# Kernel tuning notes

Measured on AMD Instinct MI355X. Metric: run time of the kernel, lower is better.

## Reference

```python
import jax, jax.numpy as jnp
import numpy as np

# dims: batch B, seq T, d_model C, expert_hidden H, n_experts E (top-1 routing)
B, T, C, H, E = 1, 256, 1024, 2048, 8
STD = 0.02


def setup_inputs() -> dict:
    key = jax.random.key(0)
    ks = jax.random.split(key, 8)
    f32 = jnp.float32
    return {
        "x": jax.random.normal(ks[0], (B, T, C), f32),
        "up": jax.random.normal(ks[1], (E, H, C), f32) * STD,
        "gate": jax.random.normal(ks[2], (E, H, C), f32) * STD,
        "down": jax.random.normal(ks[3], (E, C, H), f32) * STD,
        "router": jax.random.normal(ks[4], (E, C), f32) * STD,
        "w_up_s": jax.random.normal(ks[5], (H, C), f32) * STD,
        "w_gate_s": jax.random.normal(ks[6], (H, C), f32) * STD,
        "w_down_s": jax.random.normal(ks[7], (C, H), f32) * STD,
    }


def reference(x, up, gate, down, router, w_up_s, w_gate_s, w_down_s):
    b, t, c = x.shape
    x_ = x.reshape(b * t, c)                      # [BT, C]
    # top-1 router (gates are implicitly 1.0)
    logits = x_ @ router.T                        # [BT, E]
    idx = jnp.argmax(logits, axis=-1)             # [BT]
    onehot = jax.nn.one_hot(idx, router.shape[0], dtype=x.dtype)  # [BT, E]
    # dense all-expert SwiGLU, combined with one-hot (same math as per-token gather)
    u = jnp.einsum('bc,ehc->ebh', x_, up)         # [E, BT, H]
    g = jnp.einsum('bc,ehc->ebh', x_, gate)       # [E, BT, H]
    h = jax.nn.silu(g) * u                        # [E, BT, H]
    ye = jnp.einsum('ebh,ech->ebc', h, down)      # [E, BT, C]
    y = jnp.einsum('ebc,be->bc', ye, onehot)      # [BT, C]
    # shared expert residual
    ys = (jax.nn.silu(x_ @ w_gate_s.T) * (x_ @ w_up_s.T)) @ w_down_s.T
    return (y + ys).reshape(b, t, c)
```

## Files before the change

### kernel.cpp

```cpp
#include <hip/hip_runtime.h>
#include <hip/hip_bf16.h>

#define T_TOK 256
#define C_DIM 1024
#define H_DIM 2048
#define E_NUM 8
#define BN 64

typedef __attribute__((ext_vector_type(4))) float f32x4;
typedef __attribute__((ext_vector_type(8))) short short8;

#define WS_IDX   0
#define WS_CNT   1024
#define WS_LIST  2048
#define WS_HBUF  16384
#define WS_HSBUF (16384 + 1048576)
#define WS_YS    (16384 + 2*1048576)

__device__ __forceinline__ ushort f2bf(float f) {
    __hip_bfloat16 h = __float2bfloat16(f);
    return *reinterpret_cast<ushort*>(&h);
}

__device__ __forceinline__ short8 pack8(float4 a, float4 b) {
    short8 s;
    s[0] = (short)f2bf(a.x); s[1] = (short)f2bf(a.y);
    s[2] = (short)f2bf(a.z); s[3] = (short)f2bf(a.w);
    s[4] = (short)f2bf(b.x); s[5] = (short)f2bf(b.y);
    s[6] = (short)f2bf(b.z); s[7] = (short)f2bf(b.w);
    return s;
}

__global__ __launch_bounds__(256) void router_kernel(
    const float* __restrict__ x, const float* __restrict__ router,
    int* __restrict__ idx, int* __restrict__ cnt, int* __restrict__ list)
{
    const int t = blockIdx.x;
    const int tid = threadIdx.x;
    float4 xv = reinterpret_cast<const float4*>(x + (size_t)t * C_DIM)[tid];
    float p[E_NUM];
#pragma unroll
    for (int e = 0; e < E_NUM; e++) {
        float4 rv = reinterpret_cast<const float4*>(router + (size_t)e * C_DIM)[tid];
        p[e] = xv.x * rv.x + xv.y * rv.y + xv.z * rv.z + xv.w * rv.w;
    }
#pragma unroll
    for (int e = 0; e < E_NUM; e++) {
#pragma unroll
        for (int off = 32; off >= 1; off >>= 1)
            p[e] += __shfl_down(p[e], off, 64);
    }
    __shared__ float red[E_NUM][4];
    const int lane = tid & 63, wv = tid >> 6;
    if (lane == 0) {
#pragma unroll
        for (int e = 0; e < E_NUM; e++) red[e][wv] = p[e];
    }
    __syncthreads();
    if (tid == 0) {
        float best = -3.4e38f; int bi = 0;
#pragma unroll
        for (int e = 0; e < E_NUM; e++) {
            float v = red[e][0] + red[e][1] + red[e][2] + red[e][3];
            if (v > best) { best = v; bi = e; }
        }
        idx[t] = bi;
        int pos = atomicAdd(&cnt[bi], 1);
        list[bi * T_TOK + pos] = t;
    }
}

__global__ __launch_bounds__(256, 3) void ug_mfma(
    const float* __restrict__ x, const float* __restrict__ up, const float* __restrict__ gate,
    const float* __restrict__ w_up_s, const float* __restrict__ w_gate_s,
    const int* __restrict__ cnt, const int* __restrict__ list,
    ushort* __restrict__ hbuf, ushort* __restrict__ hsbuf)
{
    const int e = blockIdx.x;
    const bool sh = (e == E_NUM);
    const int n = sh ? T_TOK : cnt[e];
    const int tg0 = blockIdx.z * 64;
    if (tg0 >= n) return;

    const int tid = threadIdx.x;
    const int lane = tid & 63, wv = tid >> 6;

    __shared__ ushort Ax[64][72];
    __shared__ ushort Wu[64][72];
    __shared__ ushort Wg[64][72];
    __shared__ int toks_s[64];
    if (tid < 64) {
        int t = tg0 + tid;
        toks_s[tid] = (t < n) ? (sh ? t : list[e * T_TOK + t]) : -1;
    }
    __syncthreads();

    const int srow = tid >> 2;
    const int sseg = (tid & 3) * 16;
    const float* __restrict__ pu = (sh ? w_up_s   : up   + (size_t)e * H_DIM * C_DIM)
                                   + (size_t)(blockIdx.y * BN + srow) * C_DIM + sseg;
    const float* __restrict__ pg = (sh ? w_gate_s : gate + (size_t)e * H_DIM * C_DIM)
                                   + (size_t)(blockIdx.y * BN + srow) * C_DIM + sseg;
    const int stok = toks_s[srow];
    const float* __restrict__ px = x + (size_t)(stok < 0 ? 0 : stok) * C_DIM + sseg;

    float4 ru[4], rg[4], rx[4];
#define UG_LOAD(kc) do { \
        _Pragma("unroll") \
        for (int i = 0; i < 4; i++) { \
            ru[i] = *reinterpret_cast<const float4*>(pu + (kc) + i * 4); \
            rg[i] = *reinterpret_cast<const float4*>(pg + (kc) + i * 4); \
            rx[i] = (stok >= 0) ? *reinterpret_cast<const float4*>(px + (kc) + i * 4) \
                                : float4{0.f, 0.f, 0.f, 0.f}; \
        } \
    } while (0)

    const int klane = (lane >> 4) * 8;
    const int mrow = lane & 15;
    f32x4 au[4] = {{0,0,0,0},{0,0,0,0},{0,0,0,0},{0,0,0,0}};
    f32x4 ag[4] = {{0,0,0,0},{0,0,0,0},{0,0,0,0},{0,0,0,0}};

    UG_LOAD(0);
#pragma unroll 1
    for (int t = 0; t < 16; t++) {
        __syncthreads();
        *reinterpret_cast<short8*>(&Wu[srow][sseg])     = pack8(ru[0], ru[1]);
        *reinterpret_cast<short8*>(&Wu[srow][sseg + 8]) = pack8(ru[2], ru[3]);
        *reinterpret_cast<short8*>(&Wg[srow][sseg])     = pack8(rg[0], rg[1]);
        *reinterpret_cast<short8*>(&Wg[srow][sseg + 8]) = pack8(rg[2], rg[3]);
        *reinterpret_cast<short8*>(&Ax[srow][sseg])     = pack8(rx[0], rx[1]);
        *reinterpret_cast<short8*>(&Ax[srow][sseg + 8]) = pack8(rx[2], rx[3]);
        __syncthreads();
        if (t < 15) UG_LOAD((t + 1) * 64);
#pragma unroll
        for (int k0 = 0; k0 < 64; k0 += 32) {
            short8 bu = *reinterpret_cast<const short8*>(&Wu[wv * 16 + mrow][klane + k0]);
            short8 bg = *reinterpret_cast<const short8*>(&Wg[wv * 16 + mrow][klane + k0]);
#pragma unroll
            for (int mf = 0; mf < 4; mf++) {
                short8 a = *reinterpret_cast<const short8*>(&Ax[mf * 16 + mrow][klane + k0]);
                au[mf] = __builtin_amdgcn_mfma_f32_16x16x32_bf16(a, bu, au[mf], 0, 0, 0);
                ag[mf] = __builtin_amdgcn_mfma_f32_16x16x32_bf16(a, bg, ag[mf], 0, 0, 0);
            }
        }
    }
#undef UG_LOAD

    const int hglob = blockIdx.y * BN + wv * 16 + mrow;
    ushort* __restrict__ outp = sh ? hsbuf : hbuf;
#pragma unroll
    for (int mf = 0; mf < 4; mf++) {
#pragma unroll
        for (int r = 0; r < 4; r++) {
            int m = mf * 16 + (lane >> 4) * 4 + r;
            int tok = toks_s[m];
            if (tok >= 0) {
                float g = ag[mf][r], u = au[mf][r];
                float hv = u * (g / (1.f + __expf(-g)));
                outp[(size_t)tok * H_DIM + hglob] = f2bf(hv);
            }
        }
    }
}

__global__ __launch_bounds__(256, 4) void down_mfma(
    const float* __restrict__ dwn, const float* __restrict__ w_down_s,
    const ushort* __restrict__ hbuf, const ushort* __restrict__ hsbuf,
    const int* __restrict__ cnt, const int* __restrict__ list,
    float* __restrict__ y, float* __restrict__ ysbuf)
{
    const int e = blockIdx.x;
    const bool sh = (e == E_NUM);
    const int n = sh ? T_TOK : cnt[e];
    const int tg0 = blockIdx.z * 32;
    if (tg0 >= n) return;

    const int tid = threadIdx.x;
    const int lane = tid & 63, wv = tid >> 6;

    __shared__ ushort Ah[32][72];
    __shared__ ushort Wd[64][72];
    __shared__ int toks_s[32];
    if (tid < 32) {
        int t = tg0 + tid;
        toks_s[tid] = (t < n) ? (sh ? t : list[e * T_TOK + t]) : -1;
    }
    __syncthreads();

    const int srow = tid >> 2;
    const int sseg = (tid & 3) * 16;
    const float* __restrict__ pd = (sh ? w_down_s : dwn + (size_t)e * C_DIM * H_DIM)
                                   + (size_t)(blockIdx.y * BN + srow) * H_DIM + sseg;
    const int hrow = tid >> 3;
    const int hseg = (tid & 7) * 8;
    const int stok = toks_s[hrow];
    const ushort* __restrict__ hin = sh ? hsbuf : hbuf;
    const ushort* __restrict__ ph = hin + (size_t)(stok < 0 ? 0 : stok) * H_DIM + hseg;

    float4 rd[4]; short8 rh;
#define DN_LOAD(kc) do { \
        _Pragma("unroll") \
        for (int i = 0; i < 4; i++) \
            rd[i] = *reinterpret_cast<const float4*>(pd + (kc) + i * 4); \
        rh = (stok >= 0) ? *reinterpret_cast<const short8*>(ph + (kc)) \
                         : short8{0,0,0,0,0,0,0,0}; \
    } while (0)

    const int klane = (lane >> 4) * 8;
    const int mrow = lane & 15;
    f32x4 acc[2] = {{0,0,0,0},{0,0,0,0}};

    DN_LOAD(0);
#pragma unroll 1
    for (int t = 0; t < 32; t++) {
        __syncthreads();
        *reinterpret_cast<short8*>(&Wd[srow][sseg])     = pack8(rd[0], rd[1]);
        *reinterpret_cast<short8*>(&Wd[srow][sseg + 8]) = pack8(rd[2], rd[3]);
        *reinterpret_cast<short8*>(&Ah[hrow][hseg])     = rh;
        __syncthreads();
        if (t < 31) DN_LOAD((t + 1) * 64);
#pragma unroll
        for (int k0 = 0; k0 < 64; k0 += 32) {
            short8 bd = *reinterpret_cast<const short8*>(&Wd[wv * 16 + mrow][klane + k0]);
#pragma unroll
            for (int mf = 0; mf < 2; mf++) {
                short8 a = *reinterpret_cast<const short8*>(&Ah[mf * 16 + mrow][klane + k0]);
                acc[mf] = __builtin_amdgcn_mfma_f32_16x16x32_bf16(a, bd, acc[mf], 0, 0, 0);
            }
        }
    }
#undef DN_LOAD

    const int cglob = blockIdx.y * BN + wv * 16 + mrow;
    float* __restrict__ outp = sh ? ysbuf : y;
#pragma unroll
    for (int mf = 0; mf < 2; mf++) {
#pragma unroll
        for (int r = 0; r < 4; r++) {
            int m = mf * 16 + (lane >> 4) * 4 + r;
            int tok = toks_s[m];
            if (tok >= 0) outp[(size_t)tok * C_DIM + cglob] = acc[mf][r];
        }
    }
}

__global__ __launch_bounds__(256) void add_kernel(float* __restrict__ y, const float* __restrict__ ys)
{
    int i = blockIdx.x * 256 + threadIdx.x;
    float4 a = reinterpret_cast<float4*>(y)[i];
    float4 b = reinterpret_cast<const float4*>(ys)[i];
    a.x += b.x; a.y += b.y; a.z += b.z; a.w += b.w;
    reinterpret_cast<float4*>(y)[i] = a;
}

extern "C" void kernel_launch(void* const* d_in, const int* in_sizes, int n_in,
                              void* d_out, int out_size, void* d_ws, size_t ws_size,
                              hipStream_t stream)
{
    const float* x        = (const float*)d_in[0];
    const float* up       = (const float*)d_in[1];
    const float* gate     = (const float*)d_in[2];
    const float* dwn      = (const float*)d_in[3];
    const float* router   = (const float*)d_in[4];
    const float* w_up_s   = (const float*)d_in[5];
    const float* w_gate_s = (const float*)d_in[6];
    const float* w_down_s = (const float*)d_in[7];

    char* ws = (char*)d_ws;
    int* idx     = (int*)(ws + WS_IDX);
    int* cnt     = (int*)(ws + WS_CNT);
    int* list    = (int*)(ws + WS_LIST);
    ushort* hbuf  = (ushort*)(ws + WS_HBUF);
    ushort* hsbuf = (ushort*)(ws + WS_HSBUF);
    float* ysbuf  = (float*)(ws + WS_YS);
    float* y = (float*)d_out;

    hipMemsetAsync(cnt, 0, E_NUM * sizeof(int), stream);
    router_kernel<<<T_TOK, 256, 0, stream>>>(x, router, idx, cnt, list);
    ug_mfma<<<dim3(E_NUM + 1, H_DIM / BN, 4), 256, 0, stream>>>(
        x, up, gate, w_up_s, w_gate_s, cnt, list, hbuf, hsbuf);
    down_mfma<<<dim3(E_NUM + 1, C_DIM / BN, 8), 256, 0, stream>>>(
        dwn, w_down_s, hbuf, hsbuf, cnt, list, y, ysbuf);
    add_kernel<<<(T_TOK * C_DIM / 4) / 256, 256, 0, stream>>>(y, ysbuf);
}
```

Before: 101.5 us.

## Replace LDS-tiled MoE GEMMs with split-K direct-register MFMA and pre-converted bf16 activations

The router kernel now also writes a bf16 copy of x, so the up/gate GEMM no longer converts activations on every tile. Both expert GEMMs drop the LDS-staged, double-synchronised 64-wide tiles. Each block now covers 16 output columns by 32 tokens, with its four waves splitting K and loading operands straight from global memory into MFMA registers. The partial sums are then reduced through LDS. This gives far more blocks and removes the per-step barriers, at the cost of reading weights once per 32-token group and losing LDS reuse of activations.

```diff
diff --git a/kernel.cpp b/kernel.cpp
--- a/kernel.cpp
+++ b/kernel.cpp
@@ -5,17 +5,16 @@
 #define C_DIM 1024
 #define H_DIM 2048
 #define E_NUM 8
-#define BN 64
 
 typedef __attribute__((ext_vector_type(4))) float f32x4;
 typedef __attribute__((ext_vector_type(8))) short short8;
 
-#define WS_IDX   0
-#define WS_CNT   1024
-#define WS_LIST  2048
-#define WS_HBUF  16384
-#define WS_HSBUF (16384 + 1048576)
-#define WS_YS    (16384 + 2*1048576)
+#define WS_CNT    0
+#define WS_LIST   1024
+#define WS_XBF    16384
+#define WS_HBUF   (1u<<20)
+#define WS_HSBUF  (2u<<20)
+#define WS_YS     (3u<<20)
 
 __device__ __forceinline__ ushort f2bf(float f) {
     __hip_bfloat16 h = __float2bfloat16(f);
@@ -31,13 +30,19 @@
     return s;
 }
 
+#define MFMA(a, b, c) __builtin_amdgcn_mfma_f32_16x16x32_bf16((a), (b), (c), 0, 0, 0)
+
 __global__ __launch_bounds__(256) void router_kernel(
     const float* __restrict__ x, const float* __restrict__ router,
-    int* __restrict__ idx, int* __restrict__ cnt, int* __restrict__ list)
+    int* __restrict__ cnt, int* __restrict__ list, ushort* __restrict__ xbf)
 {
     const int t = blockIdx.x;
     const int tid = threadIdx.x;
     float4 xv = reinterpret_cast<const float4*>(x + (size_t)t * C_DIM)[tid];
+    ushort4 xb;
+    xb.x = f2bf(xv.x); xb.y = f2bf(xv.y); xb.z = f2bf(xv.z); xb.w = f2bf(xv.w);
+    *reinterpret_cast<ushort4*>(xbf + (size_t)t * C_DIM + tid * 4) = xb;
+
     float p[E_NUM];
 #pragma unroll
     for (int e = 0; e < E_NUM; e++) {
@@ -64,100 +69,86 @@
             float v = red[e][0] + red[e][1] + red[e][2] + red[e][3];
             if (v > best) { best = v; bi = e; }
         }
-        idx[t] = bi;
         int pos = atomicAdd(&cnt[bi], 1);
         list[bi * T_TOK + pos] = t;
     }
 }
 
-__global__ __launch_bounds__(256, 3) void ug_mfma(
-    const float* __restrict__ x, const float* __restrict__ up, const float* __restrict__ gate,
+__global__ __launch_bounds__(256, 4) void ug_mfma(
+    const ushort* __restrict__ xbf, const float* __restrict__ up, const float* __restrict__ gate,
     const float* __restrict__ w_up_s, const float* __restrict__ w_gate_s,
     const int* __restrict__ cnt, const int* __restrict__ list,
     ushort* __restrict__ hbuf, ushort* __restrict__ hsbuf)
 {
-    const int e = blockIdx.x;
+    const int e = blockIdx.x, by = blockIdx.y, tt = blockIdx.z;
     const bool sh = (e == E_NUM);
     const int n = sh ? T_TOK : cnt[e];
-    const int tg0 = blockIdx.z * 64;
-    if (tg0 >= n) return;
-
-    const int tid = threadIdx.x;
-    const int lane = tid & 63, wv = tid >> 6;
-
-    __shared__ ushort Ax[64][72];
-    __shared__ ushort Wu[64][72];
-    __shared__ ushort Wg[64][72];
-    __shared__ int toks_s[64];
-    if (tid < 64) {
-        int t = tg0 + tid;
+    if (tt * 32 >= n) return;
+    const int tid = threadIdx.x, lane = tid & 63, wv = tid >> 6;
+    const int col = lane & 15, kg = lane >> 4, kl = kg * 8;
+
+    __shared__ float red[4][2][64][4];
+    __shared__ int toks_s[32];
+    if (tid < 32) {
+        int t = tt * 32 + tid;
         toks_s[tid] = (t < n) ? (sh ? t : list[e * T_TOK + t]) : -1;
     }
     __syncthreads();
 
-    const int srow = tid >> 2;
-    const int sseg = (tid & 3) * 16;
+    const int h0 = by * 16;
+    const int kb = wv * 256;
     const float* __restrict__ pu = (sh ? w_up_s   : up   + (size_t)e * H_DIM * C_DIM)
-                                   + (size_t)(blockIdx.y * BN + srow) * C_DIM + sseg;
+                                   + (size_t)(h0 + col) * C_DIM + kb + kl;
     const float* __restrict__ pg = (sh ? w_gate_s : gate + (size_t)e * H_DIM * C_DIM)
-                                   + (size_t)(blockIdx.y * BN + srow) * C_DIM + sseg;
-    const int stok = toks_s[srow];
-    const float* __restrict__ px = x + (size_t)(stok < 0 ? 0 : stok) * C_DIM + sseg;
-
-    float4 ru[4], rg[4], rx[4];
-#define UG_LOAD(kc) do { \
-        _Pragma("unroll") \
-        for (int i = 0; i < 4; i++) { \
-            ru[i] = *reinterpret_cast<const float4*>(pu + (kc) + i * 4); \
-            rg[i] = *reinterpret_cast<const float4*>(pg + (kc) + i * 4); \
-            rx[i] = (stok >= 0) ? *reinterpret_cast<const float4*>(px + (kc) + i * 4) \
-                                : float4{0.f, 0.f, 0.f, 0.f}; \
-        } \
-    } while (0)
-
-    const int klane = (lane >> 4) * 8;
-    const int mrow = lane & 15;
-    f32x4 au[4] = {{0,0,0,0},{0,0,0,0},{0,0,0,0},{0,0,0,0}};
-    f32x4 ag[4] = {{0,0,0,0},{0,0,0,0},{0,0,0,0},{0,0,0,0}};
-
-    UG_LOAD(0);
-#pragma unroll 1
-    for (int t = 0; t < 16; t++) {
-        __syncthreads();
-        *reinterpret_cast<short8*>(&Wu[srow][sseg])     = pack8(ru[0], ru[1]);
-        *reinterpret_cast<short8*>(&Wu[srow][sseg + 8]) = pack8(ru[2], ru[3]);
-        *reinterpret_cast<short8*>(&Wg[srow][sseg])     = pack8(rg[0], rg[1]);
-        *reinterpret_cast<short8*>(&Wg[srow][sseg + 8]) = pack8(rg[2], rg[3]);
-        *reinterpret_cast<short8*>(&Ax[srow][sseg])     = pack8(rx[0], rx[1]);
-        *reinterpret_cast<short8*>(&Ax[srow][sseg + 8]) = pack8(rx[2], rx[3]);
-        __syncthreads();
-        if (t < 15) UG_LOAD((t + 1) * 64);
-#pragma unroll
-        for (int k0 = 0; k0 < 64; k0 += 32) {
-            short8 bu = *reinterpret_cast<const short8*>(&Wu[wv * 16 + mrow][klane + k0]);
-            short8 bg = *reinterpret_cast<const short8*>(&Wg[wv * 16 + mrow][klane + k0]);
-#pragma unroll
-            for (int mf = 0; mf < 4; mf++) {
-                short8 a = *reinterpret_cast<const short8*>(&Ax[mf * 16 + mrow][klane + k0]);
-                au[mf] = __builtin_amdgcn_mfma_f32_16x16x32_bf16(a, bu, au[mf], 0, 0, 0);
-                ag[mf] = __builtin_amdgcn_mfma_f32_16x16x32_bf16(a, bg, ag[mf], 0, 0, 0);
-            }
-        }
-    }
-#undef UG_LOAD
-
-    const int hglob = blockIdx.y * BN + wv * 16 + mrow;
-    ushort* __restrict__ outp = sh ? hsbuf : hbuf;
-#pragma unroll
-    for (int mf = 0; mf < 4; mf++) {
-#pragma unroll
-        for (int r = 0; r < 4; r++) {
-            int m = mf * 16 + (lane >> 4) * 4 + r;
-            int tok = toks_s[m];
+                                   + (size_t)(h0 + col) * C_DIM + kb + kl;
+    const int t0 = toks_s[col], t1 = toks_s[16 + col];
+    const ushort* __restrict__ pa0 = xbf + (size_t)(t0 < 0 ? 0 : t0) * C_DIM + kb + kl;
+    const ushort* __restrict__ pa1 = xbf + (size_t)(t1 < 0 ? 0 : t1) * C_DIM + kb + kl;
+
+    f32x4 au0 = {0,0,0,0}, au1 = {0,0,0,0}, ag0 = {0,0,0,0}, ag1 = {0,0,0,0};
+#pragma unroll 4
+    for (int k = 0; k < 8; k++) {
+        const int o = k * 32;
+        short8 a0 = *reinterpret_cast<const short8*>(pa0 + o);
+        short8 a1 = *reinterpret_cast<const short8*>(pa1 + o);
+        float4 ua = *reinterpret_cast<const float4*>(pu + o);
+        float4 ub = *reinterpret_cast<const float4*>(pu + o + 4);
+        float4 ga = *reinterpret_cast<const float4*>(pg + o);
+        float4 gb = *reinterpret_cast<const float4*>(pg + o + 4);
+        short8 bu = pack8(ua, ub), bg = pack8(ga, gb);
+        au0 = MFMA(a0, bu, au0); au1 = MFMA(a1, bu, au1);
+        ag0 = MFMA(a0, bg, ag0); ag1 = MFMA(a1, bg, ag1);
+    }
+
+    *reinterpret_cast<f32x4*>(red[wv][0][lane]) = au0;
+    *reinterpret_cast<f32x4*>(red[wv][1][lane]) = au1;
+    __syncthreads();
+    f32x4 u4 = {0,0,0,0}, g4 = {0,0,0,0};
+    const int rv = (tid >> 6) & 1, rl = tid & 63;
+    if (tid < 128) {
+        u4 = *reinterpret_cast<const f32x4*>(red[0][rv][rl]);
+        u4 += *reinterpret_cast<const f32x4*>(red[1][rv][rl]);
+        u4 += *reinterpret_cast<const f32x4*>(red[2][rv][rl]);
+        u4 += *reinterpret_cast<const f32x4*>(red[3][rv][rl]);
+    }
+    __syncthreads();
+    *reinterpret_cast<f32x4*>(red[wv][0][lane]) = ag0;
+    *reinterpret_cast<f32x4*>(red[wv][1][lane]) = ag1;
+    __syncthreads();
+    if (tid < 128) {
+        g4 = *reinterpret_cast<const f32x4*>(red[0][rv][rl]);
+        g4 += *reinterpret_cast<const f32x4*>(red[1][rv][rl]);
+        g4 += *reinterpret_cast<const f32x4*>(red[2][rv][rl]);
+        g4 += *reinterpret_cast<const f32x4*>(red[3][rv][rl]);
+        ushort* __restrict__ outp = sh ? hsbuf : hbuf;
+#pragma unroll
+        for (int j = 0; j < 4; j++) {
+            int row = (rv ? 16 : 0) + (rl >> 4) * 4 + j;
+            int tok = toks_s[row];
             if (tok >= 0) {
-                float g = ag[mf][r], u = au[mf][r];
+                float g = g4[j], u = u4[j];
                 float hv = u * (g / (1.f + __expf(-g)));
-                outp[(size_t)tok * H_DIM + hglob] = f2bf(hv);
+                outp[(size_t)tok * H_DIM + h0 + (rl & 15)] = f2bf(hv);
             }
         }
     }
@@ -167,79 +158,61 @@
     const float* __restrict__ dwn, const float* __restrict__ w_down_s,
     const ushort* __restrict__ hbuf, const ushort* __restrict__ hsbuf,
     const int* __restrict__ cnt, const int* __restrict__ list,
-    float* __restrict__ y, float* __restrict__ ysbuf)
-{
-    const int e = blockIdx.x;
+    float* __restrict__ y, float* __restrict__ yspart)
+{
+    const int e = blockIdx.x, by = blockIdx.y, tt = blockIdx.z;
     const bool sh = (e == E_NUM);
     const int n = sh ? T_TOK : cnt[e];
-    const int tg0 = blockIdx.z * 32;
-    if (tg0 >= n) return;
-
-    const int tid = threadIdx.x;
-    const int lane = tid & 63, wv = tid >> 6;
-
-    __shared__ ushort Ah[32][72];
-    __shared__ ushort Wd[64][72];
+    if (tt * 32 >= n) return;
+    const int tid = threadIdx.x, lane = tid & 63, wv = tid >> 6;
+    const int col = lane & 15, kg = lane >> 4, kl = kg * 8;
+
+    __shared__ float red[4][2][64][4];
     __shared__ int toks_s[32];
     if (tid < 32) {
-        int t = tg0 + tid;
+        int t = tt * 32 + tid;
         toks_s[tid] = (t < n) ? (sh ? t : list[e * T_TOK + t]) : -1;
     }
     __syncthreads();
 
-    const int srow = tid >> 2;
-    const int sseg = (tid & 3) * 16;
+    const int c0 = by * 16;
+    const int kb = wv * 512;
     const float* __restrict__ pd = (sh ? w_down_s : dwn + (size_t)e * C_DIM * H_DIM)
-                                   + (size_t)(blockIdx.y * BN + srow) * H_DIM + sseg;
-    const int hrow = tid >> 3;
-    const int hseg = (tid & 7) * 8;
-    const int stok = toks_s[hrow];
+                                   + (size_t)(c0 + col) * H_DIM + kb + kl;
+    const int t0 = toks_s[col], t1 = toks_s[16 + col];
     const ushort* __restrict__ hin = sh ? hsbuf : hbuf;
-    const ushort* __restrict__ ph = hin + (size_t)(stok < 0 ? 0 : stok) * H_DIM + hseg;
-
-    float4 rd[4]; short8 rh;
-#define DN_LOAD(kc) do { \
-        _Pragma("unroll") \
-        for (int i = 0; i < 4; i++) \
-            rd[i] = *reinterpret_cast<const float4*>(pd + (kc) + i * 4); \
-        rh = (stok >= 0) ? *reinterpret_cast<const short8*>(ph + (kc)) \
-                         : short8{0,0,0,0,0,0,0,0}; \
-    } while (0)
-
-    const int klane = (lane >> 4) * 8;
-    const int mrow = lane & 15;
-    f32x4 acc[2] = {{0,0,0,0},{0,0,0,0}};
-
-    DN_LOAD(0);
-#pragma unroll 1
-    for (int t = 0; t < 32; t++) {
-        __syncthreads();
-        *reinterpret_cast<short8*>(&Wd[srow][sseg])     = pack8(rd[0], rd[1]);
-        *reinterpret_cast<short8*>(&Wd[srow][sseg + 8]) = pack8(rd[2], rd[3]);
-        *reinterpret_cast<short8*>(&Ah[hrow][hseg])     = rh;
-        __syncthreads();
-        if (t < 31) DN_LOAD((t + 1) * 64);
-#pragma unroll
-        for (int k0 = 0; k0 < 64; k0 += 32) {
-            short8 bd = *reinterpret_cast<const short8*>(&Wd[wv * 16 + mrow][klane + k0]);
-#pragma unroll
-            for (int mf = 0; mf < 2; mf++) {
-                short8 a = *reinterpret_cast<const short8*>(&Ah[mf * 16 + mrow][klane + k0]);
-                acc[mf] = __builtin_amdgcn_mfma_f32_16x16x32_bf16(a, bd, acc[mf], 0, 0, 0);
-            }
-        }
-    }
-#undef DN_LOAD
-
-    const int cglob = blockIdx.y * BN + wv * 16 + mrow;
-    float* __restrict__ outp = sh ? ysbuf : y;
-#pragma unroll
-    for (int mf = 0; mf < 2; mf++) {
-#pragma unroll
-        for (int r = 0; r < 4; r++) {
-            int m = mf * 16 + (lane >> 4) * 4 + r;
-            int tok = toks_s[m];
-            if (tok >= 0) outp[(size_t)tok * C_DIM + cglob] = acc[mf][r];
+    const ushort* __restrict__ pa0 = hin + (size_t)(t0 < 0 ? 0 : t0) * H_DIM + kb + kl;
+    const ushort* __restrict__ pa1 = hin + (size_t)(t1 < 0 ? 0 : t1) * H_DIM + kb + kl;
+
+    f32x4 ac0 = {0,0,0,0}, ac1 = {0,0,0,0};
+#pragma unroll 4
+    for (int k = 0; k < 16; k++) {
+        const int o = k * 32;
+        short8 a0 = *reinterpret_cast<const short8*>(pa0 + o);
+        short8 a1 = *reinterpret_cast<const short8*>(pa1 + o);
+        float4 da = *reinterpret_cast<const float4*>(pd + o);
+        float4 db = *reinterpret_cast<const float4*>(pd + o + 4);
+        short8 bd = pack8(da, db);
+        ac0 = MFMA(a0, bd, ac0);
+        ac1 = MFMA(a1, bd, ac1);
+    }
+
+    *reinterpret_cast<f32x4*>(red[wv][0][lane]) = ac0;
+    *reinterpret_cast<f32x4*>(red[wv][1][lane]) = ac1;
+    __syncthreads();
+    const int rv = (tid >> 6) & 1, rl = tid & 63;
+    if (tid < 128) {
+        f32x4 y4;
+        y4  = *reinterpret_cast<const f32x4*>(red[0][rv][rl]);
+        y4 += *reinterpret_cast<const f32x4*>(red[1][rv][rl]);
+        y4 += *reinterpret_cast<const f32x4*>(red[2][rv][rl]);
+        y4 += *reinterpret_cast<const f32x4*>(red[3][rv][rl]);
+        float* __restrict__ outp = sh ? yspart : y;
+#pragma unroll
+        for (int j = 0; j < 4; j++) {
+            int row = (rv ? 16 : 0) + (rl >> 4) * 4 + j;
+            int tok = toks_s[row];
+            if (tok >= 0) outp[(size_t)tok * C_DIM + c0 + (rl & 15)] = y4[j];
         }
     }
 }
@@ -267,19 +240,19 @@
     const float* w_down_s = (const float*)d_in[7];
 
     char* ws = (char*)d_ws;
-    int* idx     = (int*)(ws + WS_IDX);
-    int* cnt     = (int*)(ws + WS_CNT);
-    int* list    = (int*)(ws + WS_LIST);
+    int* cnt      = (int*)(ws + WS_CNT);
+    int* list     = (int*)(ws + WS_LIST);
+    ushort* xbf   = (ushort*)(ws + WS_XBF);
     ushort* hbuf  = (ushort*)(ws + WS_HBUF);
     ushort* hsbuf = (ushort*)(ws + WS_HSBUF);
-    float* ysbuf  = (float*)(ws + WS_YS);
+    float* yspart = (float*)(ws + WS_YS);
     float* y = (float*)d_out;
 
     hipMemsetAsync(cnt, 0, E_NUM * sizeof(int), stream);
-    router_kernel<<<T_TOK, 256, 0, stream>>>(x, router, idx, cnt, list);
-    ug_mfma<<<dim3(E_NUM + 1, H_DIM / BN, 4), 256, 0, stream>>>(
-        x, up, gate, w_up_s, w_gate_s, cnt, list, hbuf, hsbuf);
-    down_mfma<<<dim3(E_NUM + 1, C_DIM / BN, 8), 256, 0, stream>>>(
-        dwn, w_down_s, hbuf, hsbuf, cnt, list, y, ysbuf);
-    add_kernel<<<(T_TOK * C_DIM / 4) / 256, 256, 0, stream>>>(y, ysbuf);
-}
+    router_kernel<<<T_TOK, 256, 0, stream>>>(x, router, cnt, list, xbf);
+    ug_mfma<<<dim3(E_NUM + 1, H_DIM / 16, 8), 256, 0, stream>>>(
+        xbf, up, gate, w_up_s, w_gate_s, cnt, list, hbuf, hsbuf);
+    down_mfma<<<dim3(E_NUM + 1, C_DIM / 16, 8), 256, 0, stream>>>(
+        dwn, w_down_s, hbuf, hsbuf, cnt, list, y, yspart);
+    add_kernel<<<(T_TOK * C_DIM / 4) / 256, 256, 0, stream>>>(y, yspart);
+}
```

New measurement: 114.5 us. 12.8% more time.
